# Kernel tuning notes

Measured on AMD Instinct MI355X. Metric: run time of the kernel, lower is better.

The kernel has to match this reference:

```python
import jax, jax.numpy as jnp
import numpy as np
import math

NUM_HEADS = 16
SIZE = 1024
HEAD_SIZE = SIZE // NUM_HEADS
B, S = 2, 2048


def setup_inputs() -> dict:
    key = jax.random.key(0)
    ks = jax.random.split(key, 11)
    sc = 1.0 / math.sqrt(SIZE)
    inp = {
        "q": jax.random.normal(ks[0], (B, S, SIZE), dtype=jnp.float32),
        "k": jax.random.normal(ks[1], (B, S, SIZE), dtype=jnp.float32),
        "v": jax.random.normal(ks[2], (B, S, SIZE), dtype=jnp.float32),
        "Wq": jax.random.normal(ks[3], (SIZE, SIZE), dtype=jnp.float32) * sc,
        "bq": jax.random.normal(ks[4], (SIZE,), dtype=jnp.float32) * sc,
        "Wk": jax.random.normal(ks[5], (SIZE, SIZE), dtype=jnp.float32) * sc,
        "bk": jax.random.normal(ks[6], (SIZE,), dtype=jnp.float32) * sc,
        "Wv": jax.random.normal(ks[7], (SIZE, SIZE), dtype=jnp.float32) * sc,
        "bv": jax.random.normal(ks[8], (SIZE,), dtype=jnp.float32) * sc,
        "Wo": jax.random.normal(ks[9], (SIZE, SIZE), dtype=jnp.float32) * sc,
        "bo": jax.random.normal(ks[10], (SIZE,), dtype=jnp.float32) * sc,
    }
    return inp


def _split_heads(x):
    # [B, S, SIZE] -> [B, H, S, D]
    b, s, _ = x.shape
    return x.reshape(b, s, NUM_HEADS, HEAD_SIZE).transpose(0, 2, 1, 3)


def reference(q, k, v, Wq, bq, Wk, bk, Wv, bv, Wo, bo):
    qh = _split_heads(q @ Wq.T + bq) / math.sqrt(HEAD_SIZE)  # [B,H,S,D]
    kh = _split_heads(k @ Wk.T + bk)
    vh = _split_heads(v @ Wv.T + bv)
    scores = jnp.einsum("bhqd,bhkd->bhqk", qh, kh)  # [B,H,S,S]
    attn = jax.nn.softmax(scores, axis=-1)
    ctx = jnp.einsum("bhqk,bhkd->bhqd", attn, vh)  # [B,H,S,D]
    ctx = ctx.transpose(0, 2, 1, 3).reshape(q.shape[0], -1, SIZE)
    return ctx @ Wo.T + bo
```

## Files before the change

### kernel.cpp

```cpp
#include <hip/hip_runtime.h>
#include <hip/hip_bf16.h>

#define SIZE 1024
#define NH 16
#define HD 64
#define BB 2
#define SS 2048
#define MROWS (BB * SS)
#define QT 128
#define NQT (SS / QT)

using bf16 = __hip_bfloat16;
using frag16 = __attribute__((ext_vector_type(8))) short;
using f32x4 = __attribute__((ext_vector_type(4))) float;
typedef unsigned int u32;

__device__ __forceinline__ void glds16(const bf16* g, bf16* l) {
    __builtin_amdgcn_global_load_lds(
        (const __attribute__((address_space(1))) u32*)g,
        (__attribute__((address_space(3))) u32*)l, 16, 0, 0);
}

__device__ __forceinline__ void cvt_store8(bf16* dst, const float* src) {
    float4 a = *(const float4*)src;
    float4 b = *(const float4*)(src + 4);
    bf16 t[8];
    t[0] = __float2bfloat16(a.x); t[1] = __float2bfloat16(a.y);
    t[2] = __float2bfloat16(a.z); t[3] = __float2bfloat16(a.w);
    t[4] = __float2bfloat16(b.x); t[5] = __float2bfloat16(b.y);
    t[6] = __float2bfloat16(b.z); t[7] = __float2bfloat16(b.w);
    *(uint4*)dst = *(const uint4*)t;
}

__global__ __launch_bounds__(256) void cast_kernel(
    const float* __restrict__ Wq, const float* __restrict__ Wk,
    const float* __restrict__ Wv, const float* __restrict__ Wo,
    const float* __restrict__ q, const float* __restrict__ k,
    const float* __restrict__ v,
    bf16* __restrict__ Wb, bf16* __restrict__ qb,
    bf16* __restrict__ kb, bf16* __restrict__ vb)
{
    const int z = blockIdx.z;
    const float* s; bf16* d; int n;
    switch (z) {
        case 0: s = Wq; d = Wb;                   n = SIZE * SIZE;  break;
        case 1: s = Wk; d = Wb + SIZE * SIZE;     n = SIZE * SIZE;  break;
        case 2: s = Wv; d = Wb + 2 * SIZE * SIZE; n = SIZE * SIZE;  break;
        case 3: s = Wo; d = Wb + 3 * SIZE * SIZE; n = SIZE * SIZE;  break;
        case 4: s = q;  d = qb;                   n = MROWS * SIZE; break;
        case 5: s = k;  d = kb;                   n = MROWS * SIZE; break;
        default: s = v; d = vb;                   n = MROWS * SIZE; break;
    }
    const int i = (blockIdx.x * 256 + threadIdx.x) * 8;
    if (i < n) cvt_store8(d + i, s + i);
}

template <typename YT>
__device__ __forceinline__ void gemm_body(
    const bf16* __restrict__ X, const bf16* __restrict__ W,
    const float* __restrict__ bias, YT* __restrict__ Y, float scale, bool vt_mode)
{
    __shared__ __align__(16) bf16 smem[8704];
    bf16* As = smem;
    bf16* Bs = smem + 4096;

    const int tid = threadIdx.x;
    const int wave = tid >> 6;
    const int lane = tid & 63;
    const int lane15 = lane & 15;
    const int quad = lane >> 4;
    const int bm = blockIdx.y * 128;
    const int bn = blockIdx.x * 128;
    const int wm = (wave & 1) * 64;
    const int wn = (wave >> 1) * 64;

    f32x4 acc[4][4];
#pragma unroll
    for (int i = 0; i < 4; i++)
#pragma unroll
        for (int j = 0; j < 4; j++)
            acc[i][j] = (f32x4){0.f, 0.f, 0.f, 0.f};

    const int srow = lane >> 2;
    const int scol = (lane & 3) * 8;

    for (int kt = 0; kt < SIZE / 32; kt++) {
        const int k0 = kt * 32;
        __syncthreads();
#pragma unroll
        for (int n = 0; n < 2; n++) {
            const int c = wave * 2 + n;
            glds16(X + (size_t)(bm + c * 16 + srow) * SIZE + k0 + scol, As + c * 512);
            glds16(W + (size_t)(bn + c * 16 + srow) * SIZE + k0 + scol, Bs + c * 512);
        }
        __syncthreads();

        frag16 a[4], b[4];
#pragma unroll
        for (int mi = 0; mi < 4; mi++)
            a[mi] = *(const frag16*)(As + (wm + mi * 16 + lane15) * 32 + quad * 8);
#pragma unroll
        for (int ni = 0; ni < 4; ni++)
            b[ni] = *(const frag16*)(Bs + (wn + ni * 16 + lane15) * 32 + quad * 8);
#pragma unroll
        for (int mi = 0; mi < 4; mi++)
#pragma unroll
            for (int ni = 0; ni < 4; ni++)
                acc[mi][ni] = __builtin_amdgcn_mfma_f32_16x16x32_bf16(
                    a[mi], b[ni], acc[mi][ni], 0, 0, 0);
    }

    if (!vt_mode) {
#pragma unroll
        for (int ni = 0; ni < 4; ni++) {
            const int col = bn + wn + ni * 16 + lane15;
            const float bv = bias[col];
#pragma unroll
            for (int mi = 0; mi < 4; mi++) {
                const int row = bm + wm + mi * 16 + quad * 4;
#pragma unroll
                for (int r = 0; r < 4; r++) {
                    float val = (acc[mi][ni][r] + bv) * scale;
                    Y[(size_t)(row + r) * SIZE + col] = (YT)val;
                }
            }
        }
    } else {
        bf16* tr = smem;
        const int bloc = bm >> 11;
        const int s0g = bm & (SS - 1);
#pragma unroll
        for (int p = 0; p < 2; p++) {
            __syncthreads();
            if ((wave >> 1) == p) {
#pragma unroll
                for (int ni = 0; ni < 4; ni++) {
                    const int colp = ni * 16 + lane15;
                    const float bv = bias[bn + p * 64 + colp];
#pragma unroll
                    for (int mi = 0; mi < 4; mi++) {
                        const int row = wm + mi * 16 + quad * 4;
#pragma unroll
                        for (int r = 0; r < 4; r++)
                            tr[colp * 136 + row + r] =
                                __float2bfloat16(acc[mi][ni][r] + bv);
                    }
                }
            }
            __syncthreads();
            const int colp = tid >> 2;
            const int gcol = bn + p * 64 + colp;
            const int hh = gcol >> 6, dd = gcol & (HD - 1);
            bf16* dst = (bf16*)Y + ((size_t)(bloc * NH + hh) * HD + dd) * SS
                        + s0g + (tid & 3) * 32;
            const bf16* src = tr + colp * 136 + (tid & 3) * 32;
#pragma unroll
            for (int j = 0; j < 4; j++)
                *(uint4*)(dst + j * 8) = *(const uint4*)(src + j * 8);
        }
    }
}

__global__ __launch_bounds__(256) void qkv_proj_kernel(
    const bf16* __restrict__ qb, const bf16* __restrict__ kb, const bf16* __restrict__ vb,
    const bf16* __restrict__ Wb,
    const float* __restrict__ bq, const float* __restrict__ bk, const float* __restrict__ bv,
    bf16* __restrict__ qh, bf16* __restrict__ kh, bf16* __restrict__ vt)
{
    const bf16 *X, *W; const float* bi; bf16* Y; float sc; bool vm;
    if (blockIdx.z == 0)      { X = qb; W = Wb;                   bi = bq; Y = qh; sc = 0.125f; vm = false; }
    else if (blockIdx.z == 1) { X = kb; W = Wb + SIZE * SIZE;     bi = bk; Y = kh; sc = 1.0f;   vm = false; }
    else                      { X = vb; W = Wb + 2 * SIZE * SIZE; bi = bv; Y = vt; sc = 1.0f;   vm = true;  }
    gemm_body<bf16>(X, W, bi, Y, sc, vm);
}

__global__ __launch_bounds__(256) void out_proj_kernel(
    const bf16* __restrict__ ctx, const bf16* __restrict__ Wob,
    const float* __restrict__ bo, float* __restrict__ out)
{
    gemm_body<float>(ctx, Wob, bo, out, 1.0f, false);
}

__global__ __launch_bounds__(256) void attn_kernel(
    const bf16* __restrict__ qh, const bf16* __restrict__ kh,
    const bf16* __restrict__ vt, bf16* __restrict__ po, float* __restrict__ pl)
{
    __shared__ __align__(16) bf16 Ks[64][72];
    __shared__ __align__(16) bf16 Vs[64][72];
    __shared__ __align__(16) bf16 Ps[4][32][72];

    const int tid = threadIdx.x;
    const int wave = tid >> 6;
    const int lane = tid & 63;
    const int lane15 = lane & 15;
    const int quad = lane >> 4;

    const int b = blockIdx.z, h = blockIdx.y;
    const int qt = blockIdx.x >> 1;
    const int sh = blockIdx.x & 1;
    const int q0 = qt * QT;

    const size_t baseq = (size_t)b * SS * SIZE + (size_t)h * HD;
    const size_t basev = (size_t)(b * NH + h) * HD * SS;
    const float LOG2E = 1.44269504088896340736f;
    const float OFF = 12.0f * LOG2E;

    frag16 aq[2][2];
#pragma unroll
    for (int m = 0; m < 2; m++) {
        const int qrow = q0 + wave * 32 + m * 16 + lane15;
        const bf16* qp = qh + baseq + (size_t)qrow * SIZE + quad * 8;
        aq[m][0] = *(const frag16*)(qp);
        aq[m][1] = *(const frag16*)(qp + 32);
    }

    float l_acc[2][4];
    f32x4 ofrag[2][4];
#pragma unroll
    for (int m = 0; m < 2; m++) {
#pragma unroll
        for (int r = 0; r < 4; r++) l_acc[m][r] = 0.f;
#pragma unroll
        for (int dt = 0; dt < 4; dt++) ofrag[m][dt] = (f32x4){0.f, 0.f, 0.f, 0.f};
    }

    const int sr = tid >> 3;
    const int sc = (tid & 7) * 8;

    for (int kt = 0; kt < (SS / 2) / 64; kt++) {
        const int s0 = sh * (SS / 2) + kt * 64;
        __syncthreads();
        *(uint4*)&Ks[sr][sc]      = *(const uint4*)(kh + baseq + (size_t)(s0 + sr) * SIZE + sc);
        *(uint4*)&Ks[sr + 32][sc] = *(const uint4*)(kh + baseq + (size_t)(s0 + sr + 32) * SIZE + sc);
        *(uint4*)&Vs[sr][sc]      = *(const uint4*)(vt + basev + (size_t)sr * SS + s0 + sc);
        *(uint4*)&Vs[sr + 32][sc] = *(const uint4*)(vt + basev + (size_t)(sr + 32) * SS + s0 + sc);
        __syncthreads();

#pragma unroll
        for (int m = 0; m < 2; m++) {
#pragma unroll
            for (int nt = 0; nt < 4; nt++) {
                f32x4 c = (f32x4){0.f, 0.f, 0.f, 0.f};
                c = __builtin_amdgcn_mfma_f32_16x16x32_bf16(
                    aq[m][0], *(const frag16*)&Ks[nt * 16 + lane15][quad * 8], c, 0, 0, 0);
                c = __builtin_amdgcn_mfma_f32_16x16x32_bf16(
                    aq[m][1], *(const frag16*)&Ks[nt * 16 + lane15][32 + quad * 8], c, 0, 0, 0);
#pragma unroll
                for (int r = 0; r < 4; r++) {
                    float p = exp2f(fminf(c[r], 30.f) * LOG2E - OFF);
                    l_acc[m][r] += p;
                    Ps[wave][m * 16 + quad * 4 + r][nt * 16 + lane15] = __float2bfloat16(p);
                }
            }
        }
        __builtin_amdgcn_wave_barrier();

        frag16 ap[2][2];
#pragma unroll
        for (int m = 0; m < 2; m++)
#pragma unroll
            for (int c2 = 0; c2 < 2; c2++)
                ap[m][c2] = *(const frag16*)&Ps[wave][m * 16 + lane15][c2 * 32 + quad * 8];

#pragma unroll
        for (int dt = 0; dt < 4; dt++) {
            frag16 bv0 = *(const frag16*)&Vs[dt * 16 + lane15][quad * 8];
            frag16 bv1 = *(const frag16*)&Vs[dt * 16 + lane15][32 + quad * 8];
#pragma unroll
            for (int m = 0; m < 2; m++) {
                ofrag[m][dt] = __builtin_amdgcn_mfma_f32_16x16x32_bf16(ap[m][0], bv0, ofrag[m][dt], 0, 0, 0);
                ofrag[m][dt] = __builtin_amdgcn_mfma_f32_16x16x32_bf16(ap[m][1], bv1, ofrag[m][dt], 0, 0, 0);
            }
        }
    }

    const int pb = ((b * NH + h) * NQT + qt) * 2 + sh;
#pragma unroll
    for (int m = 0; m < 2; m++)
#pragma unroll
        for (int r = 0; r < 4; r++) {
            float t = l_acc[m][r];
#pragma unroll
            for (int off = 1; off < 16; off <<= 1)
                t += __shfl_xor(t, off, 16);
            l_acc[m][r] = t;
        }
    if (lane15 == 0) {
        float* plp = pl + (size_t)pb * QT;
#pragma unroll
        for (int m = 0; m < 2; m++)
#pragma unroll
            for (int r = 0; r < 4; r++)
                plp[wave * 32 + m * 16 + quad * 4 + r] = l_acc[m][r];
    }
    bf16* pop = po + (size_t)pb * QT * HD;
#pragma unroll
    for (int m = 0; m < 2; m++)
#pragma unroll
        for (int dt = 0; dt < 4; dt++)
#pragma unroll
            for (int r = 0; r < 4; r++)
                pop[(size_t)(wave * 32 + m * 16 + quad * 4 + r) * HD + dt * 16 + lane15] =
                    __float2bfloat16(ofrag[m][dt][r]);
}

__global__ __launch_bounds__(256) void combine_kernel(
    const bf16* __restrict__ po, const float* __restrict__ pl, bf16* __restrict__ ctx)
{
    const int b = blockIdx.z, h = blockIdx.y, qt = blockIdx.x;
    const int tile = (b * NH + h) * NQT + qt;
    const bf16* p0 = po + (size_t)(tile * 2 + 0) * QT * HD;
    const bf16* p1 = po + (size_t)(tile * 2 + 1) * QT * HD;
    const int qr = threadIdx.x >> 1;
    const int dh = (threadIdx.x & 1) * 32;
    const float l = pl[(size_t)(tile * 2) * QT + qr] + pl[(size_t)(tile * 2 + 1) * QT + qr];
    const float inv = 1.0f / fmaxf(l, 1e-30f);
    bf16* dst = ctx + ((size_t)b * SS + qt * QT + qr) * SIZE + h * HD + dh;
    const bf16* s0p = p0 + qr * HD + dh;
    const bf16* s1p = p1 + qr * HD + dh;
#pragma unroll
    for (int j = 0; j < 32; j += 8) {
        uint4 u0 = *(const uint4*)(s0p + j);
        uint4 u1 = *(const uint4*)(s1p + j);
        const bf16* a = (const bf16*)&u0;
        const bf16* bt = (const bf16*)&u1;
        bf16 o[8];
#pragma unroll
        for (int e = 0; e < 8; e++)
            o[e] = __float2bfloat16((__bfloat162float(a[e]) + __bfloat162float(bt[e])) * inv);
        *(uint4*)(dst + j) = *(const uint4*)o;
    }
}

extern "C" void kernel_launch(void* const* d_in, const int* in_sizes, int n_in,
                              void* d_out, int out_size, void* d_ws, size_t ws_size,
                              hipStream_t stream) {
    const float* q  = (const float*)d_in[0];
    const float* k  = (const float*)d_in[1];
    const float* v  = (const float*)d_in[2];
    const float* Wq = (const float*)d_in[3];
    const float* bq = (const float*)d_in[4];
    const float* Wk = (const float*)d_in[5];
    const float* bk = (const float*)d_in[6];
    const float* Wv = (const float*)d_in[7];
    const float* bv = (const float*)d_in[8];
    const float* Wo = (const float*)d_in[9];
    const float* bo = (const float*)d_in[10];
    float* out = (float*)d_out;

    bf16* Wb  = (bf16*)d_ws;
    bf16* qb  = Wb + (size_t)4 * SIZE * SIZE;
    bf16* kb  = qb + (size_t)MROWS * SIZE;
    bf16* vb  = kb + (size_t)MROWS * SIZE;
    bf16* qh  = vb + (size_t)MROWS * SIZE;
    bf16* kh  = qh + (size_t)MROWS * SIZE;
    bf16* vt  = kh + (size_t)MROWS * SIZE;
    bf16* po  = qb;
    bf16* ctx = vb;
    float* pl = (float*)Wb;

    cast_kernel<<<dim3(MROWS * SIZE / 2048, 1, 7), 256, 0, stream>>>(
        Wq, Wk, Wv, Wo, q, k, v, Wb, qb, kb, vb);
    qkv_proj_kernel<<<dim3(SIZE / 128, MROWS / 128, 3), 256, 0, stream>>>(
        qb, kb, vb, Wb, bq, bk, bv, qh, kh, vt);
    attn_kernel<<<dim3(NQT * 2, NH, BB), 256, 0, stream>>>(qh, kh, vt, po, pl);
    combine_kernel<<<dim3(NQT, NH, BB), 256, 0, stream>>>(po, pl, ctx);
    out_proj_kernel<<<dim3(SIZE / 128, MROWS / 128, 1), 256, 0, stream>>>(
        ctx, Wb + (size_t)3 * SIZE * SIZE, bo, out);
}
```

Before: 272.9 us.

## Fuse fp32 casts into GEMM loads and combine into output projection

Removes the separate cast kernel by having the QKV and output projections load fp32 inputs and weights directly, converting them to bf16 while staging into LDS. Register-prefetches the next K tile in both GEMMs and in the attention K/V loop. Folds the split-K combine and normalisation into the output projection's A-tile load. Computes the softmax row sums with an MFMA against a ones vector instead of scalar adds plus shuffles. This trades a global memory pass and two launches for twice the global read bytes per GEMM tile (fp32 instead of bf16), and the async global-to-LDS loads are replaced by register round trips.

```diff
diff --git a/kernel.cpp b/kernel.cpp
--- a/kernel.cpp
+++ b/kernel.cpp
@@ -9,60 +9,35 @@
 #define MROWS (BB * SS)
 #define QT 128
 #define NQT (SS / QT)
+#define NKT ((SS / 2) / 64)
 
 using bf16 = __hip_bfloat16;
 using frag16 = __attribute__((ext_vector_type(8))) short;
 using f32x4 = __attribute__((ext_vector_type(4))) float;
-typedef unsigned int u32;
-
-__device__ __forceinline__ void glds16(const bf16* g, bf16* l) {
-    __builtin_amdgcn_global_load_lds(
-        (const __attribute__((address_space(1))) u32*)g,
-        (__attribute__((address_space(3))) u32*)l, 16, 0, 0);
-}
-
-__device__ __forceinline__ void cvt_store8(bf16* dst, const float* src) {
-    float4 a = *(const float4*)src;
-    float4 b = *(const float4*)(src + 4);
+
+__device__ __forceinline__ void store8_cvt(bf16* dst, const float4* f) {
     bf16 t[8];
-    t[0] = __float2bfloat16(a.x); t[1] = __float2bfloat16(a.y);
-    t[2] = __float2bfloat16(a.z); t[3] = __float2bfloat16(a.w);
-    t[4] = __float2bfloat16(b.x); t[5] = __float2bfloat16(b.y);
-    t[6] = __float2bfloat16(b.z); t[7] = __float2bfloat16(b.w);
+    t[0] = __float2bfloat16(f[0].x); t[1] = __float2bfloat16(f[0].y);
+    t[2] = __float2bfloat16(f[0].z); t[3] = __float2bfloat16(f[0].w);
+    t[4] = __float2bfloat16(f[1].x); t[5] = __float2bfloat16(f[1].y);
+    t[6] = __float2bfloat16(f[1].z); t[7] = __float2bfloat16(f[1].w);
     *(uint4*)dst = *(const uint4*)t;
 }
 
-__global__ __launch_bounds__(256) void cast_kernel(
-    const float* __restrict__ Wq, const float* __restrict__ Wk,
-    const float* __restrict__ Wv, const float* __restrict__ Wo,
-    const float* __restrict__ q, const float* __restrict__ k,
-    const float* __restrict__ v,
-    bf16* __restrict__ Wb, bf16* __restrict__ qb,
-    bf16* __restrict__ kb, bf16* __restrict__ vb)
-{
-    const int z = blockIdx.z;
-    const float* s; bf16* d; int n;
-    switch (z) {
-        case 0: s = Wq; d = Wb;                   n = SIZE * SIZE;  break;
-        case 1: s = Wk; d = Wb + SIZE * SIZE;     n = SIZE * SIZE;  break;
-        case 2: s = Wv; d = Wb + 2 * SIZE * SIZE; n = SIZE * SIZE;  break;
-        case 3: s = Wo; d = Wb + 3 * SIZE * SIZE; n = SIZE * SIZE;  break;
-        case 4: s = q;  d = qb;                   n = MROWS * SIZE; break;
-        case 5: s = k;  d = kb;                   n = MROWS * SIZE; break;
-        default: s = v; d = vb;                   n = MROWS * SIZE; break;
-    }
-    const int i = (blockIdx.x * 256 + threadIdx.x) * 8;
-    if (i < n) cvt_store8(d + i, s + i);
-}
-
-template <typename YT>
-__device__ __forceinline__ void gemm_body(
-    const bf16* __restrict__ X, const bf16* __restrict__ W,
-    const float* __restrict__ bias, YT* __restrict__ Y, float scale, bool vt_mode)
+__global__ __launch_bounds__(256) void qkv_proj_kernel(
+    const float* __restrict__ q, const float* __restrict__ k, const float* __restrict__ v,
+    const float* __restrict__ Wq, const float* __restrict__ Wk, const float* __restrict__ Wv,
+    const float* __restrict__ bq, const float* __restrict__ bk, const float* __restrict__ bv,
+    bf16* __restrict__ qh, bf16* __restrict__ kh, bf16* __restrict__ vt)
 {
     __shared__ __align__(16) bf16 smem[8704];
     bf16* As = smem;
     bf16* Bs = smem + 4096;
+
+    const float *X, *W, *bi; bf16* Y; float scale; bool vm;
+    if (blockIdx.z == 0)      { X = q; W = Wq; bi = bq; Y = qh; scale = 0.125f; vm = false; }
+    else if (blockIdx.z == 1) { X = k; W = Wk; bi = bk; Y = kh; scale = 1.0f;   vm = false; }
+    else                      { X = v; W = Wv; bi = bv; Y = vt; scale = 1.0f;   vm = true;  }
 
     const int tid = threadIdx.x;
     const int wave = tid >> 6;
@@ -81,19 +56,32 @@
         for (int j = 0; j < 4; j++)
             acc[i][j] = (f32x4){0.f, 0.f, 0.f, 0.f};
 
-    const int srow = lane >> 2;
-    const int scol = (lane & 3) * 8;
+    const int r0 = tid >> 2, c0 = (tid & 3) * 8, r1 = r0 + 64;
+    const float* xp0 = X + (size_t)(bm + r0) * SIZE + c0;
+    const float* xp1 = X + (size_t)(bm + r1) * SIZE + c0;
+    const float* wp0 = W + (size_t)(bn + r0) * SIZE + c0;
+    const float* wp1 = W + (size_t)(bn + r1) * SIZE + c0;
+
+    float4 fx0[2], fx1[2], fw0[2], fw1[2];
+    fx0[0] = *(const float4*)(xp0); fx0[1] = *(const float4*)(xp0 + 4);
+    fx1[0] = *(const float4*)(xp1); fx1[1] = *(const float4*)(xp1 + 4);
+    fw0[0] = *(const float4*)(wp0); fw0[1] = *(const float4*)(wp0 + 4);
+    fw1[0] = *(const float4*)(wp1); fw1[1] = *(const float4*)(wp1 + 4);
 
     for (int kt = 0; kt < SIZE / 32; kt++) {
-        const int k0 = kt * 32;
-        __syncthreads();
-#pragma unroll
-        for (int n = 0; n < 2; n++) {
-            const int c = wave * 2 + n;
-            glds16(X + (size_t)(bm + c * 16 + srow) * SIZE + k0 + scol, As + c * 512);
-            glds16(W + (size_t)(bn + c * 16 + srow) * SIZE + k0 + scol, Bs + c * 512);
-        }
-        __syncthreads();
+        __syncthreads();
+        store8_cvt(As + r0 * 32 + c0, fx0);
+        store8_cvt(As + r1 * 32 + c0, fx1);
+        store8_cvt(Bs + r0 * 32 + c0, fw0);
+        store8_cvt(Bs + r1 * 32 + c0, fw1);
+        __syncthreads();
+        if (kt < SIZE / 32 - 1) {
+            const int kn = (kt + 1) * 32;
+            fx0[0] = *(const float4*)(xp0 + kn); fx0[1] = *(const float4*)(xp0 + kn + 4);
+            fx1[0] = *(const float4*)(xp1 + kn); fx1[1] = *(const float4*)(xp1 + kn + 4);
+            fw0[0] = *(const float4*)(wp0 + kn); fw0[1] = *(const float4*)(wp0 + kn + 4);
+            fw1[0] = *(const float4*)(wp1 + kn); fw1[1] = *(const float4*)(wp1 + kn + 4);
+        }
 
         frag16 a[4], b[4];
 #pragma unroll
@@ -110,19 +98,18 @@
                     a[mi], b[ni], acc[mi][ni], 0, 0, 0);
     }
 
-    if (!vt_mode) {
+    if (!vm) {
 #pragma unroll
         for (int ni = 0; ni < 4; ni++) {
             const int col = bn + wn + ni * 16 + lane15;
-            const float bv = bias[col];
+            const float bv = bi[col];
 #pragma unroll
             for (int mi = 0; mi < 4; mi++) {
                 const int row = bm + wm + mi * 16 + quad * 4;
 #pragma unroll
-                for (int r = 0; r < 4; r++) {
-                    float val = (acc[mi][ni][r] + bv) * scale;
-                    Y[(size_t)(row + r) * SIZE + col] = (YT)val;
-                }
+                for (int r = 0; r < 4; r++)
+                    Y[(size_t)(row + r) * SIZE + col] =
+                        __float2bfloat16((acc[mi][ni][r] + bv) * scale);
             }
         }
     } else {
@@ -136,7 +123,7 @@
 #pragma unroll
                 for (int ni = 0; ni < 4; ni++) {
                     const int colp = ni * 16 + lane15;
-                    const float bv = bias[bn + p * 64 + colp];
+                    const float bv = bi[bn + p * 64 + colp];
 #pragma unroll
                     for (int mi = 0; mi < 4; mi++) {
                         const int row = wm + mi * 16 + quad * 4;
@@ -161,26 +148,6 @@
     }
 }
 
-__global__ __launch_bounds__(256) void qkv_proj_kernel(
-    const bf16* __restrict__ qb, const bf16* __restrict__ kb, const bf16* __restrict__ vb,
-    const bf16* __restrict__ Wb,
-    const float* __restrict__ bq, const float* __restrict__ bk, const float* __restrict__ bv,
-    bf16* __restrict__ qh, bf16* __restrict__ kh, bf16* __restrict__ vt)
-{
-    const bf16 *X, *W; const float* bi; bf16* Y; float sc; bool vm;
-    if (blockIdx.z == 0)      { X = qb; W = Wb;                   bi = bq; Y = qh; sc = 0.125f; vm = false; }
-    else if (blockIdx.z == 1) { X = kb; W = Wb + SIZE * SIZE;     bi = bk; Y = kh; sc = 1.0f;   vm = false; }
-    else                      { X = vb; W = Wb + 2 * SIZE * SIZE; bi = bv; Y = vt; sc = 1.0f;   vm = true;  }
-    gemm_body<bf16>(X, W, bi, Y, sc, vm);
-}
-
-__global__ __launch_bounds__(256) void out_proj_kernel(
-    const bf16* __restrict__ ctx, const bf16* __restrict__ Wob,
-    const float* __restrict__ bo, float* __restrict__ out)
-{
-    gemm_body<float>(ctx, Wob, bo, out, 1.0f, false);
-}
-
 __global__ __launch_bounds__(256) void attn_kernel(
     const bf16* __restrict__ qh, const bf16* __restrict__ kh,
     const bf16* __restrict__ vt, bf16* __restrict__ po, float* __restrict__ pl)
@@ -214,12 +181,14 @@
         aq[m][1] = *(const frag16*)(qp + 32);
     }
 
-    float l_acc[2][4];
-    f32x4 ofrag[2][4];
+    frag16 bones;
+#pragma unroll
+    for (int e = 0; e < 8; e++) bones[e] = (short)0x3F80;
+
+    f32x4 ofrag[2][4], l_frag[2];
 #pragma unroll
     for (int m = 0; m < 2; m++) {
-#pragma unroll
-        for (int r = 0; r < 4; r++) l_acc[m][r] = 0.f;
+        l_frag[m] = (f32x4){0.f, 0.f, 0.f, 0.f};
 #pragma unroll
         for (int dt = 0; dt < 4; dt++) ofrag[m][dt] = (f32x4){0.f, 0.f, 0.f, 0.f};
     }
@@ -227,14 +196,29 @@
     const int sr = tid >> 3;
     const int sc = (tid & 7) * 8;
 
-    for (int kt = 0; kt < (SS / 2) / 64; kt++) {
-        const int s0 = sh * (SS / 2) + kt * 64;
-        __syncthreads();
-        *(uint4*)&Ks[sr][sc]      = *(const uint4*)(kh + baseq + (size_t)(s0 + sr) * SIZE + sc);
-        *(uint4*)&Ks[sr + 32][sc] = *(const uint4*)(kh + baseq + (size_t)(s0 + sr + 32) * SIZE + sc);
-        *(uint4*)&Vs[sr][sc]      = *(const uint4*)(vt + basev + (size_t)sr * SS + s0 + sc);
-        *(uint4*)&Vs[sr + 32][sc] = *(const uint4*)(vt + basev + (size_t)(sr + 32) * SS + s0 + sc);
-        __syncthreads();
+    uint4 kr0, kr1, vr0, vr1;
+    {
+        const int s0 = sh * (SS / 2);
+        kr0 = *(const uint4*)(kh + baseq + (size_t)(s0 + sr) * SIZE + sc);
+        kr1 = *(const uint4*)(kh + baseq + (size_t)(s0 + sr + 32) * SIZE + sc);
+        vr0 = *(const uint4*)(vt + basev + (size_t)sr * SS + s0 + sc);
+        vr1 = *(const uint4*)(vt + basev + (size_t)(sr + 32) * SS + s0 + sc);
+    }
+
+    for (int kt = 0; kt < NKT; kt++) {
+        __syncthreads();
+        *(uint4*)&Ks[sr][sc] = kr0;
+        *(uint4*)&Ks[sr + 32][sc] = kr1;
+        *(uint4*)&Vs[sr][sc] = vr0;
+        *(uint4*)&Vs[sr + 32][sc] = vr1;
+        __syncthreads();
+        if (kt + 1 < NKT) {
+            const int s0 = sh * (SS / 2) + (kt + 1) * 64;
+            kr0 = *(const uint4*)(kh + baseq + (size_t)(s0 + sr) * SIZE + sc);
+            kr1 = *(const uint4*)(kh + baseq + (size_t)(s0 + sr + 32) * SIZE + sc);
+            vr0 = *(const uint4*)(vt + basev + (size_t)sr * SS + s0 + sc);
+            vr1 = *(const uint4*)(vt + basev + (size_t)(sr + 32) * SS + s0 + sc);
+        }
 
 #pragma unroll
         for (int m = 0; m < 2; m++) {
@@ -248,7 +232,6 @@
 #pragma unroll
                 for (int r = 0; r < 4; r++) {
                     float p = exp2f(fminf(c[r], 30.f) * LOG2E - OFF);
-                    l_acc[m][r] += p;
                     Ps[wave][m * 16 + quad * 4 + r][nt * 16 + lane15] = __float2bfloat16(p);
                 }
             }
@@ -261,6 +244,13 @@
 #pragma unroll
             for (int c2 = 0; c2 < 2; c2++)
                 ap[m][c2] = *(const frag16*)&Ps[wave][m * 16 + lane15][c2 * 32 + quad * 8];
+
+#pragma unroll
+        for (int m = 0; m < 2; m++)
+#pragma unroll
+            for (int c2 = 0; c2 < 2; c2++)
+                l_frag[m] = __builtin_amdgcn_mfma_f32_16x16x32_bf16(
+                    ap[m][c2], bones, l_frag[m], 0, 0, 0);
 
 #pragma unroll
         for (int dt = 0; dt < 4; dt++) {
@@ -275,23 +265,13 @@
     }
 
     const int pb = ((b * NH + h) * NQT + qt) * 2 + sh;
-#pragma unroll
-    for (int m = 0; m < 2; m++)
-#pragma unroll
-        for (int r = 0; r < 4; r++) {
-            float t = l_acc[m][r];
-#pragma unroll
-            for (int off = 1; off < 16; off <<= 1)
-                t += __shfl_xor(t, off, 16);
-            l_acc[m][r] = t;
-        }
     if (lane15 == 0) {
         float* plp = pl + (size_t)pb * QT;
 #pragma unroll
         for (int m = 0; m < 2; m++)
 #pragma unroll
             for (int r = 0; r < 4; r++)
-                plp[wave * 32 + m * 16 + quad * 4 + r] = l_acc[m][r];
+                plp[wave * 32 + m * 16 + quad * 4 + r] = l_frag[m][r];
     }
     bf16* pop = po + (size_t)pb * QT * HD;
 #pragma unroll
@@ -304,31 +284,107 @@
                     __float2bfloat16(ofrag[m][dt][r]);
 }
 
-__global__ __launch_bounds__(256) void combine_kernel(
-    const bf16* __restrict__ po, const float* __restrict__ pl, bf16* __restrict__ ctx)
+__global__ __launch_bounds__(256) void out_proj_kernel(
+    const bf16* __restrict__ po, const float* __restrict__ pl,
+    const float* __restrict__ Wo, const float* __restrict__ bo,
+    float* __restrict__ out)
 {
-    const int b = blockIdx.z, h = blockIdx.y, qt = blockIdx.x;
-    const int tile = (b * NH + h) * NQT + qt;
-    const bf16* p0 = po + (size_t)(tile * 2 + 0) * QT * HD;
-    const bf16* p1 = po + (size_t)(tile * 2 + 1) * QT * HD;
-    const int qr = threadIdx.x >> 1;
-    const int dh = (threadIdx.x & 1) * 32;
-    const float l = pl[(size_t)(tile * 2) * QT + qr] + pl[(size_t)(tile * 2 + 1) * QT + qr];
-    const float inv = 1.0f / fmaxf(l, 1e-30f);
-    bf16* dst = ctx + ((size_t)b * SS + qt * QT + qr) * SIZE + h * HD + dh;
-    const bf16* s0p = p0 + qr * HD + dh;
-    const bf16* s1p = p1 + qr * HD + dh;
-#pragma unroll
-    for (int j = 0; j < 32; j += 8) {
-        uint4 u0 = *(const uint4*)(s0p + j);
-        uint4 u1 = *(const uint4*)(s1p + j);
-        const bf16* a = (const bf16*)&u0;
-        const bf16* bt = (const bf16*)&u1;
-        bf16 o[8];
-#pragma unroll
-        for (int e = 0; e < 8; e++)
-            o[e] = __float2bfloat16((__bfloat162float(a[e]) + __bfloat162float(bt[e])) * inv);
-        *(uint4*)(dst + j) = *(const uint4*)o;
+    __shared__ __align__(16) bf16 As[64 * 32];
+    __shared__ __align__(16) bf16 Bs[128 * 32];
+
+    const int tid = threadIdx.x;
+    const int wave = tid >> 6;
+    const int lane = tid & 63;
+    const int lane15 = lane & 15;
+    const int quad = lane >> 4;
+    const int bm = blockIdx.y * 64;
+    const int bn = blockIdx.x * 128;
+    const int wn = wave * 32;
+
+    f32x4 acc[4][2];
+#pragma unroll
+    for (int i = 0; i < 4; i++)
+#pragma unroll
+        for (int j = 0; j < 2; j++)
+            acc[i][j] = (f32x4){0.f, 0.f, 0.f, 0.f};
+
+    const int ar = tid >> 2, ac = (tid & 3) * 8;
+    const int gm = bm + ar;
+    const int bb = gm >> 11, s = gm & (SS - 1);
+    const int qt = s >> 7, qr = s & (QT - 1);
+    const int tbase = bb * NH * NQT + qt;
+    const int br0 = tid >> 2, bc = (tid & 3) * 8, br1 = br0 + 64;
+    const float* wp0 = Wo + (size_t)(bn + br0) * SIZE + bc;
+    const float* wp1 = Wo + (size_t)(bn + br1) * SIZE + bc;
+
+    uint4 rp0, rp1; float rinv;
+    float4 rw0[2], rw1[2];
+
+#define LOAD_A(KT)                                                              \
+    {                                                                           \
+        const int k0_ = (KT) * 32;                                              \
+        const int h_ = k0_ >> 6;                                                \
+        const size_t tile_ = (size_t)(tbase + h_ * NQT) * 2;                    \
+        const int d_ = (k0_ & 32) + ac;                                         \
+        rp0 = *(const uint4*)(po + ((tile_ + 0) * QT + qr) * HD + d_);          \
+        rp1 = *(const uint4*)(po + ((tile_ + 1) * QT + qr) * HD + d_);          \
+        const float l_ = pl[(tile_ + 0) * QT + qr] + pl[(tile_ + 1) * QT + qr]; \
+        rinv = 1.0f / fmaxf(l_, 1e-30f);                                        \
+    }
+
+    LOAD_A(0);
+    rw0[0] = *(const float4*)(wp0); rw0[1] = *(const float4*)(wp0 + 4);
+    rw1[0] = *(const float4*)(wp1); rw1[1] = *(const float4*)(wp1 + 4);
+
+    for (int kt = 0; kt < SIZE / 32; kt++) {
+        __syncthreads();
+        {
+            const bf16* a0 = (const bf16*)&rp0;
+            const bf16* a1 = (const bf16*)&rp1;
+            bf16 t[8];
+#pragma unroll
+            for (int e = 0; e < 8; e++)
+                t[e] = __float2bfloat16(
+                    (__bfloat162float(a0[e]) + __bfloat162float(a1[e])) * rinv);
+            *(uint4*)(As + ar * 32 + ac) = *(const uint4*)t;
+        }
+        store8_cvt(Bs + br0 * 32 + bc, rw0);
+        store8_cvt(Bs + br1 * 32 + bc, rw1);
+        __syncthreads();
+        if (kt < SIZE / 32 - 1) {
+            LOAD_A(kt + 1);
+            const int kn = (kt + 1) * 32;
+            rw0[0] = *(const float4*)(wp0 + kn); rw0[1] = *(const float4*)(wp0 + kn + 4);
+            rw1[0] = *(const float4*)(wp1 + kn); rw1[1] = *(const float4*)(wp1 + kn + 4);
+        }
+
+        frag16 a[4], b[2];
+#pragma unroll
+        for (int mi = 0; mi < 4; mi++)
+            a[mi] = *(const frag16*)(As + (mi * 16 + lane15) * 32 + quad * 8);
+#pragma unroll
+        for (int ni = 0; ni < 2; ni++)
+            b[ni] = *(const frag16*)(Bs + (wn + ni * 16 + lane15) * 32 + quad * 8);
+#pragma unroll
+        for (int mi = 0; mi < 4; mi++)
+#pragma unroll
+            for (int ni = 0; ni < 2; ni++)
+                acc[mi][ni] = __builtin_amdgcn_mfma_f32_16x16x32_bf16(
+                    a[mi], b[ni], acc[mi][ni], 0, 0, 0);
+    }
+#undef LOAD_A
+
+#pragma unroll
+    for (int ni = 0; ni < 2; ni++) {
+        const int col = bn + wn + ni * 16 + lane15;
+        const float bv = bo[col];
+#pragma unroll
+        for (int mi = 0; mi < 4; mi++) {
+            const int row = bm + mi * 16 + quad * 4;
+#pragma unroll
+            for (int r = 0; r < 4; r++)
+                out[(size_t)(row + r) * SIZE + col] = acc[mi][ni][r] + bv;
+        }
     }
 }
 
@@ -348,23 +404,16 @@
     const float* bo = (const float*)d_in[10];
     float* out = (float*)d_out;
 
-    bf16* Wb  = (bf16*)d_ws;
-    bf16* qb  = Wb + (size_t)4 * SIZE * SIZE;
-    bf16* kb  = qb + (size_t)MROWS * SIZE;
-    bf16* vb  = kb + (size_t)MROWS * SIZE;
-    bf16* qh  = vb + (size_t)MROWS * SIZE;
-    bf16* kh  = qh + (size_t)MROWS * SIZE;
-    bf16* vt  = kh + (size_t)MROWS * SIZE;
-    bf16* po  = qb;
-    bf16* ctx = vb;
-    float* pl = (float*)Wb;
-
-    cast_kernel<<<dim3(MROWS * SIZE / 2048, 1, 7), 256, 0, stream>>>(
-        Wq, Wk, Wv, Wo, q, k, v, Wb, qb, kb, vb);
+    bf16* qh = (bf16*)d_ws;
+    bf16* kh = qh + (size_t)MROWS * SIZE;
+    bf16* vt = kh + (size_t)MROWS * SIZE;
+    bf16* po = vt + (size_t)MROWS * SIZE;
+    float* pl = (float*)(po + (size_t)2 * MROWS * HD * NH / NH * 2);
+    pl = (float*)(po + (size_t)1024 * QT * HD);
+
     qkv_proj_kernel<<<dim3(SIZE / 128, MROWS / 128, 3), 256, 0, stream>>>(
-        qb, kb, vb, Wb, bq, bk, bv, qh, kh, vt);
+        q, k, v, Wq, Wk, Wv, bq, bk, bv, qh, kh, vt);
     attn_kernel<<<dim3(NQT * 2, NH, BB), 256, 0, stream>>>(qh, kh, vt, po, pl);
-    combine_kernel<<<dim3(NQT, NH, BB), 256, 0, stream>>>(po, pl, ctx);
-    out_proj_kernel<<<dim3(SIZE / 128, MROWS / 128, 1), 256, 0, stream>>>(
-        ctx, Wb + (size_t)3 * SIZE * SIZE, bo, out);
+    out_proj_kernel<<<dim3(SIZE / 128, MROWS / 64, 1), 256, 0, stream>>>(
+        po, pl, Wo, bo, out);
 }
```

New measurement: 288.7 us. 5.8% more time.

## Compute softmax row sums via MFMA, transpose QK tiles, split out-proj into smaller tiles

Applied to the files above, without the earlier changes.

The attention kernel now computes the score MFMA with K as the A operand, so each lane holds a row-contiguous slice of P and can write it with one packed 8-byte store. The row-sum reduction is done by an extra MFMA of P against a vector of bf16 ones instead of scalar adds plus a shuffle tree. The K fragments are hoisted out of the m loop. The output projection gets its own kernel with 64x128 tiles, giving twice as many blocks for the 4096x1024 GEMM so more CUs are busy, at the cost of less operand reuse per block.

```diff
diff --git a/kernel.cpp b/kernel.cpp
--- a/kernel.cpp
+++ b/kernel.cpp
@@ -9,6 +9,7 @@
 #define MROWS (BB * SS)
 #define QT 128
 #define NQT (SS / QT)
+#define NKT ((SS / 2) / 64)
 
 using bf16 = __hip_bfloat16;
 using frag16 = __attribute__((ext_vector_type(8))) short;
@@ -55,10 +56,9 @@
     if (i < n) cvt_store8(d + i, s + i);
 }
 
-template <typename YT>
 __device__ __forceinline__ void gemm_body(
     const bf16* __restrict__ X, const bf16* __restrict__ W,
-    const float* __restrict__ bias, YT* __restrict__ Y, float scale, bool vt_mode)
+    const float* __restrict__ bias, bf16* __restrict__ Y, float scale, bool vt_mode)
 {
     __shared__ __align__(16) bf16 smem[8704];
     bf16* As = smem;
@@ -119,10 +119,9 @@
             for (int mi = 0; mi < 4; mi++) {
                 const int row = bm + wm + mi * 16 + quad * 4;
 #pragma unroll
-                for (int r = 0; r < 4; r++) {
-                    float val = (acc[mi][ni][r] + bv) * scale;
-                    Y[(size_t)(row + r) * SIZE + col] = (YT)val;
-                }
+                for (int r = 0; r < 4; r++)
+                    Y[(size_t)(row + r) * SIZE + col] =
+                        __float2bfloat16((acc[mi][ni][r] + bv) * scale);
             }
         }
     } else {
@@ -171,14 +170,7 @@
     if (blockIdx.z == 0)      { X = qb; W = Wb;                   bi = bq; Y = qh; sc = 0.125f; vm = false; }
     else if (blockIdx.z == 1) { X = kb; W = Wb + SIZE * SIZE;     bi = bk; Y = kh; sc = 1.0f;   vm = false; }
     else                      { X = vb; W = Wb + 2 * SIZE * SIZE; bi = bv; Y = vt; sc = 1.0f;   vm = true;  }
-    gemm_body<bf16>(X, W, bi, Y, sc, vm);
-}
-
-__global__ __launch_bounds__(256) void out_proj_kernel(
-    const bf16* __restrict__ ctx, const bf16* __restrict__ Wob,
-    const float* __restrict__ bo, float* __restrict__ out)
-{
-    gemm_body<float>(ctx, Wob, bo, out, 1.0f, false);
+    gemm_body(X, W, bi, Y, sc, vm);
 }
 
 __global__ __launch_bounds__(256) void attn_kernel(
@@ -214,12 +206,14 @@
         aq[m][1] = *(const frag16*)(qp + 32);
     }
 
-    float l_acc[2][4];
-    f32x4 ofrag[2][4];
+    frag16 bones;
+#pragma unroll
+    for (int e = 0; e < 8; e++) bones[e] = (short)0x3F80;
+
+    f32x4 ofrag[2][4], l_frag[2];
 #pragma unroll
     for (int m = 0; m < 2; m++) {
-#pragma unroll
-        for (int r = 0; r < 4; r++) l_acc[m][r] = 0.f;
+        l_frag[m] = (f32x4){0.f, 0.f, 0.f, 0.f};
 #pragma unroll
         for (int dt = 0; dt < 4; dt++) ofrag[m][dt] = (f32x4){0.f, 0.f, 0.f, 0.f};
     }
@@ -227,7 +221,7 @@
     const int sr = tid >> 3;
     const int sc = (tid & 7) * 8;
 
-    for (int kt = 0; kt < (SS / 2) / 64; kt++) {
+    for (int kt = 0; kt < NKT; kt++) {
         const int s0 = sh * (SS / 2) + kt * 64;
         __syncthreads();
         *(uint4*)&Ks[sr][sc]      = *(const uint4*)(kh + baseq + (size_t)(s0 + sr) * SIZE + sc);
@@ -236,21 +230,24 @@
         *(uint4*)&Vs[sr + 32][sc] = *(const uint4*)(vt + basev + (size_t)(sr + 32) * SS + s0 + sc);
         __syncthreads();
 
+        frag16 kf[4][2];
+#pragma unroll
+        for (int nt = 0; nt < 4; nt++) {
+            kf[nt][0] = *(const frag16*)&Ks[nt * 16 + lane15][quad * 8];
+            kf[nt][1] = *(const frag16*)&Ks[nt * 16 + lane15][32 + quad * 8];
+        }
 #pragma unroll
         for (int m = 0; m < 2; m++) {
 #pragma unroll
             for (int nt = 0; nt < 4; nt++) {
                 f32x4 c = (f32x4){0.f, 0.f, 0.f, 0.f};
-                c = __builtin_amdgcn_mfma_f32_16x16x32_bf16(
-                    aq[m][0], *(const frag16*)&Ks[nt * 16 + lane15][quad * 8], c, 0, 0, 0);
-                c = __builtin_amdgcn_mfma_f32_16x16x32_bf16(
-                    aq[m][1], *(const frag16*)&Ks[nt * 16 + lane15][32 + quad * 8], c, 0, 0, 0);
-#pragma unroll
-                for (int r = 0; r < 4; r++) {
-                    float p = exp2f(fminf(c[r], 30.f) * LOG2E - OFF);
-                    l_acc[m][r] += p;
-                    Ps[wave][m * 16 + quad * 4 + r][nt * 16 + lane15] = __float2bfloat16(p);
-                }
+                c = __builtin_amdgcn_mfma_f32_16x16x32_bf16(kf[nt][0], aq[m][0], c, 0, 0, 0);
+                c = __builtin_amdgcn_mfma_f32_16x16x32_bf16(kf[nt][1], aq[m][1], c, 0, 0, 0);
+                bf16 p4[4];
+#pragma unroll
+                for (int r = 0; r < 4; r++)
+                    p4[r] = __float2bfloat16(exp2f(fminf(c[r], 30.f) * LOG2E - OFF));
+                *(uint2*)&Ps[wave][m * 16 + lane15][nt * 16 + quad * 4] = *(const uint2*)p4;
             }
         }
         __builtin_amdgcn_wave_barrier();
@@ -261,6 +258,13 @@
 #pragma unroll
             for (int c2 = 0; c2 < 2; c2++)
                 ap[m][c2] = *(const frag16*)&Ps[wave][m * 16 + lane15][c2 * 32 + quad * 8];
+
+#pragma unroll
+        for (int m = 0; m < 2; m++)
+#pragma unroll
+            for (int c2 = 0; c2 < 2; c2++)
+                l_frag[m] = __builtin_amdgcn_mfma_f32_16x16x32_bf16(
+                    ap[m][c2], bones, l_frag[m], 0, 0, 0);
 
 #pragma unroll
         for (int dt = 0; dt < 4; dt++) {
@@ -275,23 +279,13 @@
     }
 
     const int pb = ((b * NH + h) * NQT + qt) * 2 + sh;
-#pragma unroll
-    for (int m = 0; m < 2; m++)
-#pragma unroll
-        for (int r = 0; r < 4; r++) {
-            float t = l_acc[m][r];
-#pragma unroll
-            for (int off = 1; off < 16; off <<= 1)
-                t += __shfl_xor(t, off, 16);
-            l_acc[m][r] = t;
-        }
     if (lane15 == 0) {
         float* plp = pl + (size_t)pb * QT;
 #pragma unroll
         for (int m = 0; m < 2; m++)
 #pragma unroll
             for (int r = 0; r < 4; r++)
-                plp[wave * 32 + m * 16 + quad * 4 + r] = l_acc[m][r];
+                plp[wave * 32 + m * 16 + quad * 4 + r] = l_frag[m][r];
     }
     bf16* pop = po + (size_t)pb * QT * HD;
 #pragma unroll
@@ -329,6 +323,72 @@
         for (int e = 0; e < 8; e++)
             o[e] = __float2bfloat16((__bfloat162float(a[e]) + __bfloat162float(bt[e])) * inv);
         *(uint4*)(dst + j) = *(const uint4*)o;
+    }
+}
+
+__global__ __launch_bounds__(256) void out_proj_kernel(
+    const bf16* __restrict__ ctx, const bf16* __restrict__ Wob,
+    const float* __restrict__ bo, float* __restrict__ out)
+{
+    __shared__ __align__(16) bf16 As[64 * 32];
+    __shared__ __align__(16) bf16 Bs[128 * 32];
+
+    const int tid = threadIdx.x;
+    const int wave = tid >> 6;
+    const int lane = tid & 63;
+    const int lane15 = lane & 15;
+    const int quad = lane >> 4;
+    const int bm = blockIdx.y * 64;
+    const int bn = blockIdx.x * 128;
+    const int wn = wave * 32;
+
+    f32x4 acc[4][2];
+#pragma unroll
+    for (int i = 0; i < 4; i++)
+#pragma unroll
+        for (int j = 0; j < 2; j++)
+            acc[i][j] = (f32x4){0.f, 0.f, 0.f, 0.f};
+
+    const int srow = lane >> 2;
+    const int scol = (lane & 3) * 8;
+
+    for (int kt = 0; kt < SIZE / 32; kt++) {
+        const int k0 = kt * 32;
+        __syncthreads();
+        glds16(ctx + (size_t)(bm + wave * 16 + srow) * SIZE + k0 + scol, As + wave * 512);
+#pragma unroll
+        for (int n = 0; n < 2; n++) {
+            const int c = wave * 2 + n;
+            glds16(Wob + (size_t)(bn + c * 16 + srow) * SIZE + k0 + scol, Bs + c * 512);
+        }
+        __syncthreads();
+
+        frag16 a[4], b[2];
+#pragma unroll
+        for (int mi = 0; mi < 4; mi++)
+            a[mi] = *(const frag16*)(As + (mi * 16 + lane15) * 32 + quad * 8);
+#pragma unroll
+        for (int ni = 0; ni < 2; ni++)
+            b[ni] = *(const frag16*)(Bs + (wn + ni * 16 + lane15) * 32 + quad * 8);
+#pragma unroll
+        for (int mi = 0; mi < 4; mi++)
+#pragma unroll
+            for (int ni = 0; ni < 2; ni++)
+                acc[mi][ni] = __builtin_amdgcn_mfma_f32_16x16x32_bf16(
+                    a[mi], b[ni], acc[mi][ni], 0, 0, 0);
+    }
+
+#pragma unroll
+    for (int ni = 0; ni < 2; ni++) {
+        const int col = bn + wn + ni * 16 + lane15;
+        const float bv = bo[col];
+#pragma unroll
+        for (int mi = 0; mi < 4; mi++) {
+            const int row = bm + mi * 16 + quad * 4;
+#pragma unroll
+            for (int r = 0; r < 4; r++)
+                out[(size_t)(row + r) * SIZE + col] = acc[mi][ni][r] + bv;
+        }
     }
 }
 
@@ -365,6 +425,6 @@
         qb, kb, vb, Wb, bq, bk, bv, qh, kh, vt);
     attn_kernel<<<dim3(NQT * 2, NH, BB), 256, 0, stream>>>(qh, kh, vt, po, pl);
     combine_kernel<<<dim3(NQT, NH, BB), 256, 0, stream>>>(po, pl, ctx);
-    out_proj_kernel<<<dim3(SIZE / 128, MROWS / 128, 1), 256, 0, stream>>>(
+    out_proj_kernel<<<dim3(SIZE / 128, MROWS / 64, 1), 256, 0, stream>>>(
         ctx, Wb + (size_t)3 * SIZE * SIZE, bo, out);
 }
```

Result: faster. 261.2 us (-4.3%).
